# Kernel optimization log

Hardware: AMD Instinct MI355X
Metric: run time of the kernel (lower is better)

The kernel has to match this reference:

```python
import jax, jax.numpy as jnp
import numpy as np

N = 50000      # nodes
E = 1000000    # edges
NF = 5         # node_features
EF = 2         # edge_features
RS = 128       # rnn_size
RES = 32       # rnn_edge_size
H = 4          # heads
C = 16         # out_features
FIN = RS + RES # GAT in_channels
NEG_SLOPE = 0.2


def lstm_step(x, h, c, Wih, Whh, bih, bhh):
    # Single-step LSTM (torch gate order: i, f, g, o)
    g = x @ Wih.T + h @ Whh.T + bih + bhh
    i, f, gg, o = jnp.split(g, 4, axis=-1)
    i = jax.nn.sigmoid(i); f = jax.nn.sigmoid(f)
    gg = jnp.tanh(gg); o = jax.nn.sigmoid(o)
    c2 = f * c + i * gg
    return o * jnp.tanh(c2), c2


def setup_inputs() -> dict:
    key = jax.random.key(0)
    ks = jax.random.split(key, 20)
    p = lambda k, shape: (jax.random.normal(k, shape) * 0.1).astype(jnp.float32)
    return dict(
        x=jax.random.normal(ks[0], (N, NF), jnp.float32),
        edge_index=jax.random.randint(ks[1], (2, E), 0, N),
        edge_attr=jax.random.normal(ks[2], (E, EF), jnp.float32),
        h_node_h=p(ks[3], (N, RS)), h_node_c=p(ks[4], (N, RS)),
        h_edge_h=p(ks[5], (E, RES)), h_edge_c=p(ks[6], (E, RES)),
        Wih_n=p(ks[7], (4 * RS, NF)), Whh_n=p(ks[8], (4 * RS, RS)),
        bih_n=p(ks[9], (4 * RS,)), bhh_n=p(ks[10], (4 * RS,)),
        Wih_e=p(ks[11], (4 * RES, EF)), Whh_e=p(ks[12], (4 * RES, RES)),
        bih_e=p(ks[13], (4 * RES,)), bhh_e=p(ks[14], (4 * RES,)),
        W_gat=p(ks[15], (FIN, H * C)),
        att_src=p(ks[16], (H, C)), att_dst=p(ks[17], (H, C)),
        bias_gat=p(ks[18], (C,)),
    )


def reference(x, edge_index, edge_attr, h_node_h, h_node_c, h_edge_h, h_edge_c,
              Wih_n, Whh_n, bih_n, bhh_n, Wih_e, Whh_e, bih_e, bhh_e,
              W_gat, att_src, att_dst, bias_gat):
    n = x.shape[0]
    # --- edge history encoder: per-edge LSTM step + scatter-mean to dst nodes ---
    he, ce = lstm_step(edge_attr, h_edge_h, h_edge_c, Wih_e, Whh_e, bih_e, bhh_e)
    dst0 = edge_index[1]
    esum = jax.ops.segment_sum(he, dst0, num_segments=n)
    deg = jax.ops.segment_sum(jnp.ones((he.shape[0], 1), he.dtype), dst0, num_segments=n)
    edge_enc = esum / jnp.maximum(deg, 1.0)            # [N, RES]
    # --- node history encoder: per-node LSTM step ---
    hn, cn = lstm_step(x, h_node_h, h_node_c, Wih_n, Whh_n, bih_n, bhh_n)
    feat = jnp.concatenate([hn, edge_enc], axis=-1)    # [N, FIN]
    # --- GATConv (PyG v1 style, add_self_loops=True, concat=False) ---
    xl = (feat @ W_gat).reshape(n, H, C)               # [N, H, C]
    a_src = jnp.einsum('nhc,hc->nh', xl, att_src)
    a_dst = jnp.einsum('nhc,hc->nh', xl, att_dst)
    loops = jnp.arange(n)
    src = jnp.concatenate([edge_index[0], loops])
    dst = jnp.concatenate([edge_index[1], loops])
    alpha = jax.nn.leaky_relu(a_src[src] + a_dst[dst], NEG_SLOPE)  # [E+N, H]
    m = jax.ops.segment_max(alpha, dst, num_segments=n)
    ea = jnp.exp(alpha - m[dst])
    s = jax.ops.segment_sum(ea, dst, num_segments=n)
    w = ea / s[dst]                                     # segment softmax over dst
    out = jax.ops.segment_sum(xl[src] * w[:, :, None], dst, num_segments=n)  # [N,H,C]
    out = out.mean(axis=1) + bias_gat                   # concat=False -> head mean
    return (out, hn, cn, he, ce)
```

## Files before the change

kernel.cpp:

```cpp
#include <hip/hip_runtime.h>

#define CAP 128

typedef __attribute__((ext_vector_type(8))) short bf16x8;
typedef __attribute__((ext_vector_type(4))) float f32x4;

__device__ __forceinline__ float sigf(float x) {
    return __builtin_amdgcn_rcpf(1.0f + __expf(-x));
}
__device__ __forceinline__ float tanhfast(float x) {
    return 2.0f * __builtin_amdgcn_rcpf(1.0f + __expf(-2.0f * x)) - 1.0f;
}
__device__ __forceinline__ short bfr(float f) {
    unsigned u = __float_as_uint(f);
    unsigned r = (u + 0x7FFFu + ((u >> 16) & 1u)) >> 16;
    return (short)r;
}
__device__ __forceinline__ float bf2f(unsigned short u) {
    return __uint_as_float(((unsigned)u) << 16);
}
__device__ __forceinline__ bf16x8 cvt8(const float* p) {
    const float4* q = (const float4*)p;
    float4 u = q[0], v = q[1];
    bf16x8 r;
    r[0]=bfr(u.x); r[1]=bfr(u.y); r[2]=bfr(u.z); r[3]=bfr(u.w);
    r[4]=bfr(v.x); r[5]=bfr(v.y); r[6]=bfr(v.z); r[7]=bfr(v.w);
    return r;
}

__global__ void convert_kernel(
    const float* __restrict__ Whh_n, const float* __restrict__ Wih_n,
    const float* __restrict__ bih_n, const float* __restrict__ bhh_n,
    const float* __restrict__ Whh_e, const float* __restrict__ Wih_e,
    const float* __restrict__ bih_e, const float* __restrict__ bhh_e,
    const float* __restrict__ Wgat,
    unsigned short* __restrict__ WnF, unsigned short* __restrict__ WeF,
    unsigned short* __restrict__ WgF, int* __restrict__ cnt, int N)
{
    int i = blockIdx.x * 256 + threadIdx.x;
    if (i < N) cnt[i] = 0;
    if (i < 512 * 160) {
        int j = i & 7, unit = i >> 3;
        int lane = unit & 63, tk = unit >> 6;
        int t = tk / 5, k4 = tk - t * 5;
        int r = t * 16 + (lane & 15);
        int k = k4 * 32 + (lane >> 4) * 8 + j;
        float v = (k < 128) ? Whh_n[r * 128 + k]
                : (k < 133) ? Wih_n[r * 5 + (k - 128)]
                : (k == 133) ? (bih_n[r] + bhh_n[r]) : 0.f;
        WnF[i] = (unsigned short)bfr(v);
    }
    if (i < 128 * 64) {
        int j = i & 7, unit = i >> 3;
        int lane = unit & 63, ts = unit >> 6;
        int t = ts >> 1, s = ts & 1;
        int r = t * 16 + (lane & 15);
        int k = s * 32 + (lane >> 4) * 8 + j;
        float v = (k < 32) ? Whh_e[r * 32 + k]
                : (k < 34) ? Wih_e[r * 2 + (k - 32)]
                : (k == 34) ? (bih_e[r] + bhh_e[r]) : 0.f;
        WeF[i] = (unsigned short)bfr(v);
    }
    if (i < 64 * 160) {
        int j = i & 7, unit = i >> 3;
        int lane = unit & 63, tk = unit >> 6;
        int t = tk / 5, k4 = tk - t * 5;
        int r = t * 16 + (lane & 15);
        int k = k4 * 32 + (lane >> 4) * 8 + j;
        WgF[i] = (unsigned short)bfr(Wgat[k * 64 + r]);
    }
}

__global__ void csr_fill_kernel(const int* __restrict__ dst, int* __restrict__ cnt,
                                int* __restrict__ eid, int E)
{
    int e = blockIdx.x * blockDim.x + threadIdx.x;
    if (e >= E) return;
    int d = dst[e];
    int k = atomicAdd(cnt + d, 1);
    if (k < CAP) eid[(size_t)d * CAP + k] = e;
}

__global__ __launch_bounds__(256) void edge_lstm_mfma(
    const float* __restrict__ eattr, const float* __restrict__ h_in, const float* __restrict__ c_in,
    const unsigned short* __restrict__ WeF,
    float* __restrict__ he_out, float* __restrict__ ce_out, int E)
{
    const int lane = threadIdx.x & 63, wave = threadIdx.x >> 6;
    const int lr = lane & 15, lg = lane >> 4;
    const int T = E >> 4;
    const int wstride = gridDim.x * 4;
    const int wid = blockIdx.x * 4 + wave;
    if (wid >= T) return;
    const bf16x8* Wv = (const bf16x8*)WeF;
    bf16x8 wa0[8], wa1[8];
    #pragma unroll
    for (int t = 0; t < 8; ++t) {
        wa0[t] = Wv[(t * 2 + 0) * 64 + lane];
        wa1[t] = Wv[(t * 2 + 1) * 64 + lane];
    }
    const int jb0 = lg * 4, jb1 = 16 + lg * 4;
    float4 ph0, ph1; f32x4 pc0, pc1; float2 pea;
    {
        const int e0 = wid * 16 + lr;
        const float4* hp = (const float4*)(h_in + (size_t)e0 * 32);
        ph0 = hp[lg * 2]; ph1 = hp[lg * 2 + 1];
        pc0 = *(const f32x4*)(c_in + (size_t)e0 * 32 + jb0);
        pc1 = *(const f32x4*)(c_in + (size_t)e0 * 32 + jb1);
        pea = *(const float2*)(eattr + (size_t)e0 * 2);
    }
    for (int t = wid; t < T; t += wstride) {
        const float4 h0 = ph0, h1 = ph1; const f32x4 c0v = pc0, c1v = pc1; const float2 ea = pea;
        const int edge = t * 16 + lr;
        const int tn = t + wstride;
        if (tn < T) {
            const int en = tn * 16 + lr;
            const float4* hp = (const float4*)(h_in + (size_t)en * 32);
            ph0 = hp[lg * 2]; ph1 = hp[lg * 2 + 1];
            pc0 = *(const f32x4*)(c_in + (size_t)en * 32 + jb0);
            pc1 = *(const f32x4*)(c_in + (size_t)en * 32 + jb1);
            pea = *(const float2*)(eattr + (size_t)en * 2);
        }
        bf16x8 b0;
        b0[0]=bfr(h0.x); b0[1]=bfr(h0.y); b0[2]=bfr(h0.z); b0[3]=bfr(h0.w);
        b0[4]=bfr(h1.x); b0[5]=bfr(h1.y); b0[6]=bfr(h1.z); b0[7]=bfr(h1.w);
        bf16x8 b1 = {0,0,0,0,0,0,0,0};
        if (lg == 0) {
            b1[0] = bfr(ea.x); b1[1] = bfr(ea.y); b1[2] = (short)0x3F80;
        }
        f32x4 acc[8];
        #pragma unroll
        for (int tt = 0; tt < 8; ++tt) {
            f32x4 v = {0, 0, 0, 0};
            v = __builtin_amdgcn_mfma_f32_16x16x32_bf16(wa0[tt], b0, v, 0, 0, 0);
            v = __builtin_amdgcn_mfma_f32_16x16x32_bf16(wa1[tt], b1, v, 0, 0, 0);
            acc[tt] = v;
        }
        #pragma unroll
        for (int u = 0; u < 2; ++u) {
            const int jb = u ? jb1 : jb0;
            const f32x4 cold = u ? c1v : c0v;
            f32x4 cres, hres;
            #pragma unroll
            for (int q = 0; q < 4; ++q) {
                float gi = acc[u][q],     gf = acc[u + 2][q];
                float gg = acc[u + 4][q], go = acc[u + 6][q];
                float c2 = sigf(gf) * cold[q] + sigf(gi) * tanhfast(gg);
                cres[q] = c2;
                hres[q] = sigf(go) * tanhfast(c2);
            }
            __builtin_nontemporal_store(cres, (f32x4*)(ce_out + (size_t)edge * 32 + jb));
            *(f32x4*)(he_out + (size_t)edge * 32 + jb) = hres;
        }
    }
}

__global__ __launch_bounds__(256) void node_lstm_mfma(
    const float* __restrict__ x, const float* __restrict__ h_in, const float* __restrict__ c_in,
    const unsigned short* __restrict__ WnF,
    float* __restrict__ hn_out, float* __restrict__ cn_out, int N)
{
    const int lane = threadIdx.x & 63, wave = threadIdx.x >> 6;
    const int n0 = blockIdx.x * 64 + wave * 16;
    if (n0 >= N) return;
    const int lr = lane & 15, lg = lane >> 4;
    const int node = n0 + lr;
    bf16x8 b[5];
    const float* hp = h_in + (size_t)node * 128 + lg * 8;
    b[0] = cvt8(hp); b[1] = cvt8(hp + 32); b[2] = cvt8(hp + 64); b[3] = cvt8(hp + 96);
    bf16x8 bx = {0,0,0,0,0,0,0,0};
    if (lg == 0) {
        const float* xp = x + (size_t)node * 5;
        bx[0]=bfr(xp[0]); bx[1]=bfr(xp[1]); bx[2]=bfr(xp[2]); bx[3]=bfr(xp[3]); bx[4]=bfr(xp[4]);
        bx[5] = (short)0x3F80;
    }
    b[4] = bx;
    const bf16x8* Wv = (const bf16x8*)WnF;
    f32x4 acc[32];
    #pragma unroll
    for (int t = 0; t < 32; ++t) {
        const bf16x8* ap = Wv + t * 320 + lane;
        f32x4 v = {0, 0, 0, 0};
        #pragma unroll
        for (int k4 = 0; k4 < 5; ++k4)
            v = __builtin_amdgcn_mfma_f32_16x16x32_bf16(ap[k4 * 64], b[k4], v, 0, 0, 0);
        acc[t] = v;
    }
    #pragma unroll
    for (int u = 0; u < 8; ++u) {
        const int jb = u * 16 + lg * 4;
        f32x4 cold = *(const f32x4*)(c_in + (size_t)node * 128 + jb);
        f32x4 cres, hres;
        #pragma unroll
        for (int q = 0; q < 4; ++q) {
            float gi = acc[u][q],        gf = acc[u + 8][q];
            float gg = acc[u + 16][q],   go = acc[u + 24][q];
            float c2 = sigf(gf) * cold[q] + sigf(gi) * tanhfast(gg);
            cres[q] = c2;
            hres[q] = sigf(go) * tanhfast(c2);
        }
        __builtin_nontemporal_store(cres, (f32x4*)(cn_out + (size_t)node * 128 + jb));
        *(f32x4*)(hn_out + (size_t)node * 128 + jb) = hres;
    }
}

__global__ __launch_bounds__(256) void enc_gatxl_kernel(
    const int* __restrict__ cnt, const int* __restrict__ eid, const float* __restrict__ he,
    const float* __restrict__ hn, const unsigned short* __restrict__ WgF,
    const float* __restrict__ attS, const float* __restrict__ attD,
    unsigned short* __restrict__ xlb, float* __restrict__ asrc, float* __restrict__ adst, int N)
{
    __shared__ float encs[64 * 36];
    const int lane = threadIdx.x & 63, wave = threadIdx.x >> 6;
    const int nbase = blockIdx.x * 64 + wave * 16;
    if (nbase >= N) return;
    const int half = lane >> 5, hl = lane & 31;
    const int g4 = hl >> 3, l8 = hl & 7;
    for (int t = 0; t < 16; t += 2) {
        const int node = nbase + t + half;
        const int c = cnt[node];
        const int m = min(c, CAP);
        const int* el = eid + (size_t)node * CAP;
        f32x4 acc = {0, 0, 0, 0};
        for (int i = g4; i < m; i += 4)
            acc += *(const f32x4*)(he + (size_t)el[i] * 32 + l8 * 4);
        #pragma unroll
        for (int off = 8; off <= 16; off <<= 1) {
            acc[0] += __shfl_xor(acc[0], off);
            acc[1] += __shfl_xor(acc[1], off);
            acc[2] += __shfl_xor(acc[2], off);
            acc[3] += __shfl_xor(acc[3], off);
        }
        if (g4 == 0) {
            float inv = 1.0f / fmaxf((float)c, 1.0f);
            f32x4 r; r[0]=acc[0]*inv; r[1]=acc[1]*inv; r[2]=acc[2]*inv; r[3]=acc[3]*inv;
            *(f32x4*)(&encs[(wave * 16 + t + half) * 36 + l8 * 4]) = r;
        }
    }
    const int lr = lane & 15, lg = lane >> 4;
    const int node = nbase + lr;
    bf16x8 b[5];
    const float* hp = hn + (size_t)node * 128 + lg * 8;
    b[0] = cvt8(hp); b[1] = cvt8(hp + 32); b[2] = cvt8(hp + 64); b[3] = cvt8(hp + 96);
    b[4] = cvt8(&encs[(wave * 16 + lr) * 36 + lg * 8]);
    const bf16x8* Wv = (const bf16x8*)WgF;
    #pragma unroll
    for (int t = 0; t < 4; ++t) {
        const bf16x8* ap = Wv + t * 320 + lane;
        f32x4 v = {0, 0, 0, 0};
        #pragma unroll
        for (int k4 = 0; k4 < 5; ++k4)
            v = __builtin_amdgcn_mfma_f32_16x16x32_bf16(ap[k4 * 64], b[k4], v, 0, 0, 0);
        ushort4 pk;
        pk.x = (unsigned short)bfr(v[0]); pk.y = (unsigned short)bfr(v[1]);
        pk.z = (unsigned short)bfr(v[2]); pk.w = (unsigned short)bfr(v[3]);
        *(ushort4*)(xlb + (size_t)node * 64 + t * 16 + lg * 4) = pk;
        const f32x4 ws = *(const f32x4*)(attS + t * 16 + lg * 4);
        const f32x4 wd = *(const f32x4*)(attD + t * 16 + lg * 4);
        float p1 = v[0]*ws[0] + v[1]*ws[1] + v[2]*ws[2] + v[3]*ws[3];
        float p2 = v[0]*wd[0] + v[1]*wd[1] + v[2]*wd[2] + v[3]*wd[3];
        p1 += __shfl_xor(p1, 16); p2 += __shfl_xor(p2, 16);
        p1 += __shfl_xor(p1, 32); p2 += __shfl_xor(p2, 32);
        if (lg == 0) {
            asrc[(size_t)node * 4 + t] = p1;
            adst[(size_t)node * 4 + t] = p2;
        }
    }
}

__global__ __launch_bounds__(256) void gat_node_kernel(
    const int* __restrict__ cnt, const int* __restrict__ eid,
    const int* __restrict__ src_idx,
    const float* __restrict__ asrc, const float* __restrict__ adst,
    const unsigned short* __restrict__ xlb, const float* __restrict__ bias,
    float* __restrict__ out, int N)
{
    const int wid = (blockIdx.x * blockDim.x + threadIdx.x) >> 6;
    const int lane = threadIdx.x & 63;
    if (wid >= N) return;
    const int n = wid;
    const int m = min(cnt[n], CAP);
    const int h = lane >> 4, c16 = lane & 15;
    const int nslot = (m + 15) >> 4;
    const float ad = adst[n * 4 + h];
    float aself = asrc[n * 4 + h] + ad;
    aself = aself > 0.f ? aself : 0.2f * aself;
    const int* el = eid + (size_t)n * CAP;
    int   ss[8];
    float aa[8];
    float mx = aself;
    #pragma unroll
    for (int k = 0; k < 8; ++k) {
        if (k >= nslot) break;
        int i = k * 16 + c16;
        if (i < m) {
            int s = src_idx[el[i]];
            float a = asrc[s * 4 + h] + ad;
            a = a > 0.f ? a : 0.2f * a;
            ss[k] = s; aa[k] = a;
            mx = fmaxf(mx, a);
        } else { ss[k] = 0; aa[k] = -1e30f; }
    }
    #pragma unroll
    for (int off = 1; off < 16; off <<= 1) mx = fmaxf(mx, __shfl_xor(mx, off));
    float ea[8];
    float p = 0.f;
    #pragma unroll
    for (int k = 0; k < 8; ++k) {
        if (k >= nslot) break;
        ea[k] = __expf(aa[k] - mx);
        p += ea[k];
    }
    #pragma unroll
    for (int off = 1; off < 16; off <<= 1) p += __shfl_xor(p, off);
    float eself = __expf(aself - mx);
    float sacc = eself + p;
    float oacc = eself * bf2f(xlb[(size_t)n * 64 + lane]);
    const int grp = lane & 48;
    #pragma unroll
    for (int k = 0; k < 8; ++k) {
        if (k >= nslot) break;
        const int lim = min(16, m - k * 16);
        #pragma unroll 4
        for (int cc = 0; cc < lim; ++cc) {
            int srcl = grp | cc;
            float w = __shfl(ea[k], srcl);
            int   s = __shfl(ss[k], srcl);
            oacc += w * bf2f(xlb[(size_t)s * 64 + lane]);
        }
    }
    float r = oacc / sacc;
    r += __shfl_xor(r, 16);
    r += __shfl_xor(r, 32);
    if (lane < 16) out[(size_t)n * 16 + lane] = 0.25f * r + bias[lane];
}

extern "C" void kernel_launch(void* const* d_in, const int* in_sizes, int n_in,
                              void* d_out, int out_size, void* d_ws, size_t ws_size,
                              hipStream_t stream)
{
    const float* x     = (const float*)d_in[0];
    const int*   ei    = (const int*)  d_in[1];
    const float* eattr = (const float*)d_in[2];
    const float* hn_h  = (const float*)d_in[3];
    const float* hn_c  = (const float*)d_in[4];
    const float* he_h  = (const float*)d_in[5];
    const float* he_c  = (const float*)d_in[6];
    const float* Wih_n = (const float*)d_in[7];
    const float* Whh_n = (const float*)d_in[8];
    const float* bih_n = (const float*)d_in[9];
    const float* bhh_n = (const float*)d_in[10];
    const float* Wih_e = (const float*)d_in[11];
    const float* Whh_e = (const float*)d_in[12];
    const float* bih_e = (const float*)d_in[13];
    const float* bhh_e = (const float*)d_in[14];
    const float* W_gat = (const float*)d_in[15];
    const float* attS  = (const float*)d_in[16];
    const float* attD  = (const float*)d_in[17];
    const float* biasG = (const float*)d_in[18];

    const int N = in_sizes[0] / 5;
    const int E = in_sizes[2] / 2;

    float* out = (float*)d_out;
    float* hn  = out + (size_t)N * 16;
    float* cn  = hn  + (size_t)N * 128;
    float* he  = cn  + (size_t)N * 128;
    float* ce  = he  + (size_t)E * 32;

    char* p = (char*)d_ws;
    size_t off = 0;
    auto take = [&](size_t bytes) -> void* {
        void* r = p + off;
        off = (off + bytes + 255) & ~(size_t)255;
        return r;
    };
    int*   cnt  = (int*)  take((size_t)N * 4);
    int*   eid  = (int*)  take((size_t)N * CAP * 4);
    unsigned short* xlb = (unsigned short*)take((size_t)N * 64 * 2);
    float* asrc = (float*)take((size_t)N * 4 * 4);
    float* adst = (float*)take((size_t)N * 4 * 4);
    unsigned short* WnF = (unsigned short*)take(512 * 160 * 2);
    unsigned short* WeF = (unsigned short*)take(128 * 64 * 2);
    unsigned short* WgF = (unsigned short*)take(64 * 160 * 2);

    convert_kernel<<<(512 * 160 + 255) / 256, 256, 0, stream>>>(
        Whh_n, Wih_n, bih_n, bhh_n, Whh_e, Wih_e, bih_e, bhh_e, W_gat,
        WnF, WeF, WgF, cnt, N);
    csr_fill_kernel<<<(E + 255) / 256, 256, 0, stream>>>(ei + E, cnt, eid, E);
    edge_lstm_mfma<<<2048, 256, 0, stream>>>(
        eattr, he_h, he_c, WeF, he, ce, E);
    node_lstm_mfma<<<(N + 63) / 64, 256, 0, stream>>>(
        x, hn_h, hn_c, WnF, hn, cn, N);
    enc_gatxl_kernel<<<(N + 63) / 64, 256, 0, stream>>>(
        cnt, eid, he, hn, WgF, attS, attD, xlb, asrc, adst, N);
    gat_node_kernel<<<(N + 3) / 4, 256, 0, stream>>>(
        cnt, eid, ei, asrc, adst, xlb, biasG, out, N);
}
```

Baseline: 380.1 us.

## Fuse CSR fill, edge LSTM and node LSTM into one block-specialized kernel

Merges the CSR-fill atomics, the edge LSTM and the node LSTM into a single launch. The 4096 blocks are partitioned by block index: three of every four run edge LSTM work, and the remaining blocks are split between the node LSTM and the CSR fill, so these independent streams can overlap on the GPU. The node weight layout is permuted so that the four gates for each hidden slice sit next to each other. This lets the node LSTM compute and consume four accumulators at a time instead of holding 32, which lowers register pressure. The goal is to remove launch gaps and tail idling between the three kernels. The cost is that block types may be imbalanced and the fused kernel's register footprint is set by its heaviest branch.

```diff
diff --git a/kernel.cpp b/kernel.cpp
--- a/kernel.cpp
+++ b/kernel.cpp
@@ -42,8 +42,8 @@
     if (i < 512 * 160) {
         int j = i & 7, unit = i >> 3;
         int lane = unit & 63, tk = unit >> 6;
-        int t = tk / 5, k4 = tk - t * 5;
-        int r = t * 16 + (lane & 15);
+        int tp = tk / 5, k4 = tk - tp * 5;
+        int r = (tp & 3) * 128 + (tp >> 2) * 16 + (lane & 15);
         int k = k4 * 32 + (lane >> 4) * 8 + j;
         float v = (k < 128) ? Whh_n[r * 128 + k]
                 : (k < 133) ? Wih_n[r * 5 + (k - 128)]
@@ -71,136 +71,136 @@
     }
 }
 
-__global__ void csr_fill_kernel(const int* __restrict__ dst, int* __restrict__ cnt,
-                                int* __restrict__ eid, int E)
-{
-    int e = blockIdx.x * blockDim.x + threadIdx.x;
-    if (e >= E) return;
-    int d = dst[e];
-    int k = atomicAdd(cnt + d, 1);
-    if (k < CAP) eid[(size_t)d * CAP + k] = e;
-}
-
-__global__ __launch_bounds__(256) void edge_lstm_mfma(
-    const float* __restrict__ eattr, const float* __restrict__ h_in, const float* __restrict__ c_in,
+__global__ __launch_bounds__(256) void phase1_kernel(
+    const float* __restrict__ eattr, const float* __restrict__ he_h, const float* __restrict__ he_c,
     const unsigned short* __restrict__ WeF,
-    float* __restrict__ he_out, float* __restrict__ ce_out, int E)
-{
+    float* __restrict__ he_out, float* __restrict__ ce_out, int E,
+    const float* __restrict__ x, const float* __restrict__ hn_h, const float* __restrict__ hn_c,
+    const unsigned short* __restrict__ WnF,
+    float* __restrict__ hn_out, float* __restrict__ cn_out, int N,
+    const int* __restrict__ dst, int* __restrict__ cnt, int* __restrict__ eid)
+{
+    const int B = blockIdx.x;
     const int lane = threadIdx.x & 63, wave = threadIdx.x >> 6;
     const int lr = lane & 15, lg = lane >> 4;
-    const int T = E >> 4;
-    const int wstride = gridDim.x * 4;
-    const int wid = blockIdx.x * 4 + wave;
-    if (wid >= T) return;
-    const bf16x8* Wv = (const bf16x8*)WeF;
-    bf16x8 wa0[8], wa1[8];
-    #pragma unroll
-    for (int t = 0; t < 8; ++t) {
-        wa0[t] = Wv[(t * 2 + 0) * 64 + lane];
-        wa1[t] = Wv[(t * 2 + 1) * 64 + lane];
-    }
-    const int jb0 = lg * 4, jb1 = 16 + lg * 4;
-    float4 ph0, ph1; f32x4 pc0, pc1; float2 pea;
-    {
-        const int e0 = wid * 16 + lr;
-        const float4* hp = (const float4*)(h_in + (size_t)e0 * 32);
-        ph0 = hp[lg * 2]; ph1 = hp[lg * 2 + 1];
-        pc0 = *(const f32x4*)(c_in + (size_t)e0 * 32 + jb0);
-        pc1 = *(const f32x4*)(c_in + (size_t)e0 * 32 + jb1);
-        pea = *(const float2*)(eattr + (size_t)e0 * 2);
-    }
-    for (int t = wid; t < T; t += wstride) {
-        const float4 h0 = ph0, h1 = ph1; const f32x4 c0v = pc0, c1v = pc1; const float2 ea = pea;
-        const int edge = t * 16 + lr;
-        const int tn = t + wstride;
-        if (tn < T) {
-            const int en = tn * 16 + lr;
-            const float4* hp = (const float4*)(h_in + (size_t)en * 32);
+    const int r4 = B & 3;
+
+    if (r4 != 3) {
+        const int eb = (B >> 2) * 3 + r4;
+        const int T = E >> 4;
+        const int wstride = 3072 * 4;
+        const int wid = eb * 4 + wave;
+        if (wid >= T) return;
+        const bf16x8* Wv = (const bf16x8*)WeF;
+        bf16x8 wa0[8], wa1[8];
+        #pragma unroll
+        for (int t = 0; t < 8; ++t) {
+            wa0[t] = Wv[(t * 2 + 0) * 64 + lane];
+            wa1[t] = Wv[(t * 2 + 1) * 64 + lane];
+        }
+        const int jb0 = lg * 4, jb1 = 16 + lg * 4;
+        float4 ph0, ph1; f32x4 pc0, pc1; float2 pea;
+        {
+            const int e0 = wid * 16 + lr;
+            const float4* hp = (const float4*)(he_h + (size_t)e0 * 32);
             ph0 = hp[lg * 2]; ph1 = hp[lg * 2 + 1];
-            pc0 = *(const f32x4*)(c_in + (size_t)en * 32 + jb0);
-            pc1 = *(const f32x4*)(c_in + (size_t)en * 32 + jb1);
-            pea = *(const float2*)(eattr + (size_t)en * 2);
-        }
-        bf16x8 b0;
-        b0[0]=bfr(h0.x); b0[1]=bfr(h0.y); b0[2]=bfr(h0.z); b0[3]=bfr(h0.w);
-        b0[4]=bfr(h1.x); b0[5]=bfr(h1.y); b0[6]=bfr(h1.z); b0[7]=bfr(h1.w);
-        bf16x8 b1 = {0,0,0,0,0,0,0,0};
-        if (lg == 0) {
-            b1[0] = bfr(ea.x); b1[1] = bfr(ea.y); b1[2] = (short)0x3F80;
-        }
-        f32x4 acc[8];
-        #pragma unroll
-        for (int tt = 0; tt < 8; ++tt) {
-            f32x4 v = {0, 0, 0, 0};
-            v = __builtin_amdgcn_mfma_f32_16x16x32_bf16(wa0[tt], b0, v, 0, 0, 0);
-            v = __builtin_amdgcn_mfma_f32_16x16x32_bf16(wa1[tt], b1, v, 0, 0, 0);
-            acc[tt] = v;
-        }
-        #pragma unroll
-        for (int u = 0; u < 2; ++u) {
-            const int jb = u ? jb1 : jb0;
-            const f32x4 cold = u ? c1v : c0v;
-            f32x4 cres, hres;
+            pc0 = *(const f32x4*)(he_c + (size_t)e0 * 32 + jb0);
+            pc1 = *(const f32x4*)(he_c + (size_t)e0 * 32 + jb1);
+            pea = *(const float2*)(eattr + (size_t)e0 * 2);
+        }
+        for (int t = wid; t < T; t += wstride) {
+            const float4 h0 = ph0, h1 = ph1; const f32x4 c0v = pc0, c1v = pc1; const float2 ea = pea;
+            const int edge = t * 16 + lr;
+            const int tn = t + wstride;
+            if (tn < T) {
+                const int en = tn * 16 + lr;
+                const float4* hp = (const float4*)(he_h + (size_t)en * 32);
+                ph0 = hp[lg * 2]; ph1 = hp[lg * 2 + 1];
+                pc0 = *(const f32x4*)(he_c + (size_t)en * 32 + jb0);
+                pc1 = *(const f32x4*)(he_c + (size_t)en * 32 + jb1);
+                pea = *(const float2*)(eattr + (size_t)en * 2);
+            }
+            bf16x8 b0;
+            b0[0]=bfr(h0.x); b0[1]=bfr(h0.y); b0[2]=bfr(h0.z); b0[3]=bfr(h0.w);
+            b0[4]=bfr(h1.x); b0[5]=bfr(h1.y); b0[6]=bfr(h1.z); b0[7]=bfr(h1.w);
+            bf16x8 b1 = {0,0,0,0,0,0,0,0};
+            if (lg == 0) {
+                b1[0] = bfr(ea.x); b1[1] = bfr(ea.y); b1[2] = (short)0x3F80;
+            }
+            f32x4 acc[8];
             #pragma unroll
-            for (int q = 0; q < 4; ++q) {
-                float gi = acc[u][q],     gf = acc[u + 2][q];
-                float gg = acc[u + 4][q], go = acc[u + 6][q];
-                float c2 = sigf(gf) * cold[q] + sigf(gi) * tanhfast(gg);
-                cres[q] = c2;
-                hres[q] = sigf(go) * tanhfast(c2);
-            }
-            __builtin_nontemporal_store(cres, (f32x4*)(ce_out + (size_t)edge * 32 + jb));
-            *(f32x4*)(he_out + (size_t)edge * 32 + jb) = hres;
-        }
-    }
-}
-
-__global__ __launch_bounds__(256) void node_lstm_mfma(
-    const float* __restrict__ x, const float* __restrict__ h_in, const float* __restrict__ c_in,
-    const unsigned short* __restrict__ WnF,
-    float* __restrict__ hn_out, float* __restrict__ cn_out, int N)
-{
-    const int lane = threadIdx.x & 63, wave = threadIdx.x >> 6;
-    const int n0 = blockIdx.x * 64 + wave * 16;
-    if (n0 >= N) return;
-    const int lr = lane & 15, lg = lane >> 4;
-    const int node = n0 + lr;
-    bf16x8 b[5];
-    const float* hp = h_in + (size_t)node * 128 + lg * 8;
-    b[0] = cvt8(hp); b[1] = cvt8(hp + 32); b[2] = cvt8(hp + 64); b[3] = cvt8(hp + 96);
-    bf16x8 bx = {0,0,0,0,0,0,0,0};
-    if (lg == 0) {
-        const float* xp = x + (size_t)node * 5;
-        bx[0]=bfr(xp[0]); bx[1]=bfr(xp[1]); bx[2]=bfr(xp[2]); bx[3]=bfr(xp[3]); bx[4]=bfr(xp[4]);
-        bx[5] = (short)0x3F80;
-    }
-    b[4] = bx;
-    const bf16x8* Wv = (const bf16x8*)WnF;
-    f32x4 acc[32];
-    #pragma unroll
-    for (int t = 0; t < 32; ++t) {
-        const bf16x8* ap = Wv + t * 320 + lane;
-        f32x4 v = {0, 0, 0, 0};
-        #pragma unroll
-        for (int k4 = 0; k4 < 5; ++k4)
-            v = __builtin_amdgcn_mfma_f32_16x16x32_bf16(ap[k4 * 64], b[k4], v, 0, 0, 0);
-        acc[t] = v;
-    }
-    #pragma unroll
-    for (int u = 0; u < 8; ++u) {
-        const int jb = u * 16 + lg * 4;
-        f32x4 cold = *(const f32x4*)(c_in + (size_t)node * 128 + jb);
-        f32x4 cres, hres;
-        #pragma unroll
-        for (int q = 0; q < 4; ++q) {
-            float gi = acc[u][q],        gf = acc[u + 8][q];
-            float gg = acc[u + 16][q],   go = acc[u + 24][q];
-            float c2 = sigf(gf) * cold[q] + sigf(gi) * tanhfast(gg);
-            cres[q] = c2;
-            hres[q] = sigf(go) * tanhfast(c2);
-        }
-        __builtin_nontemporal_store(cres, (f32x4*)(cn_out + (size_t)node * 128 + jb));
-        *(f32x4*)(hn_out + (size_t)node * 128 + jb) = hres;
+            for (int tt = 0; tt < 8; ++tt) {
+                f32x4 v = {0, 0, 0, 0};
+                v = __builtin_amdgcn_mfma_f32_16x16x32_bf16(wa0[tt], b0, v, 0, 0, 0);
+                v = __builtin_amdgcn_mfma_f32_16x16x32_bf16(wa1[tt], b1, v, 0, 0, 0);
+                acc[tt] = v;
+            }
+            #pragma unroll
+            for (int u = 0; u < 2; ++u) {
+                const int jb = u ? jb1 : jb0;
+                const f32x4 cold = u ? c1v : c0v;
+                f32x4 cres, hres;
+                #pragma unroll
+                for (int q = 0; q < 4; ++q) {
+                    float gi = acc[u][q],     gf = acc[u + 2][q];
+                    float gg = acc[u + 4][q], go = acc[u + 6][q];
+                    float c2 = sigf(gf) * cold[q] + sigf(gi) * tanhfast(gg);
+                    cres[q] = c2;
+                    hres[q] = sigf(go) * tanhfast(c2);
+                }
+                __builtin_nontemporal_store(cres, (f32x4*)(ce_out + (size_t)edge * 32 + jb));
+                *(f32x4*)(he_out + (size_t)edge * 32 + jb) = hres;
+            }
+        }
+    } else if ((B & 7) == 3) {
+        const int nb = B >> 3;
+        const int NG = N >> 4;
+        const int wstride = 512 * 4;
+        const bf16x8* Wv = (const bf16x8*)WnF;
+        for (int gidx = nb * 4 + wave; gidx < NG; gidx += wstride) {
+            const int node = gidx * 16 + lr;
+            bf16x8 b[5];
+            const float* hp = hn_h + (size_t)node * 128 + lg * 8;
+            b[0] = cvt8(hp); b[1] = cvt8(hp + 32); b[2] = cvt8(hp + 64); b[3] = cvt8(hp + 96);
+            bf16x8 bx = {0,0,0,0,0,0,0,0};
+            if (lg == 0) {
+                const float* xp = x + (size_t)node * 5;
+                bx[0]=bfr(xp[0]); bx[1]=bfr(xp[1]); bx[2]=bfr(xp[2]); bx[3]=bfr(xp[3]); bx[4]=bfr(xp[4]);
+                bx[5] = (short)0x3F80;
+            }
+            b[4] = bx;
+            #pragma unroll
+            for (int u = 0; u < 8; ++u) {
+                f32x4 acc[4];
+                #pragma unroll
+                for (int g = 0; g < 4; ++g) {
+                    const bf16x8* ap = Wv + (u * 4 + g) * 320 + lane;
+                    f32x4 v = {0, 0, 0, 0};
+                    #pragma unroll
+                    for (int k4 = 0; k4 < 5; ++k4)
+                        v = __builtin_amdgcn_mfma_f32_16x16x32_bf16(ap[k4 * 64], b[k4], v, 0, 0, 0);
+                    acc[g] = v;
+                }
+                const int jb = u * 16 + lg * 4;
+                f32x4 cold = *(const f32x4*)(hn_c + (size_t)node * 128 + jb);
+                f32x4 cres, hres;
+                #pragma unroll
+                for (int q = 0; q < 4; ++q) {
+                    float c2 = sigf(acc[1][q]) * cold[q] + sigf(acc[0][q]) * tanhfast(acc[2][q]);
+                    cres[q] = c2;
+                    hres[q] = sigf(acc[3][q]) * tanhfast(c2);
+                }
+                __builtin_nontemporal_store(cres, (f32x4*)(cn_out + (size_t)node * 128 + jb));
+                *(f32x4*)(hn_out + (size_t)node * 128 + jb) = hres;
+            }
+        }
+    } else {
+        const int cb = B >> 3;
+        for (int e = cb * 256 + threadIdx.x; e < E; e += 512 * 256) {
+            int d = dst[e];
+            int k = atomicAdd(cnt + d, 1);
+            if (k < CAP) eid[(size_t)d * CAP + k] = e;
+        }
     }
 }
 
@@ -387,11 +387,10 @@
     convert_kernel<<<(512 * 160 + 255) / 256, 256, 0, stream>>>(
         Whh_n, Wih_n, bih_n, bhh_n, Whh_e, Wih_e, bih_e, bhh_e, W_gat,
         WnF, WeF, WgF, cnt, N);
-    csr_fill_kernel<<<(E + 255) / 256, 256, 0, stream>>>(ei + E, cnt, eid, E);
-    edge_lstm_mfma<<<2048, 256, 0, stream>>>(
-        eattr, he_h, he_c, WeF, he, ce, E);
-    node_lstm_mfma<<<(N + 63) / 64, 256, 0, stream>>>(
-        x, hn_h, hn_c, WnF, hn, cn, N);
+    phase1_kernel<<<4096, 256, 0, stream>>>(
+        eattr, he_h, he_c, WeF, he, ce, E,
+        x, hn_h, hn_c, WnF, hn, cn, N,
+        ei + E, cnt, eid);
     enc_gatxl_kernel<<<(N + 63) / 64, 256, 0, stream>>>(
         cnt, eid, he, hn, WgF, attS, attD, xlb, asrc, adst, N);
     gat_node_kernel<<<(N + 3) / 4, 256, 0, stream>>>(
```

New measurement: 930.1 us. +144.7%, slower.

## Coalesce edge LSTM I/O via LDS transpose and interleave node LSTM gates

Applied to the files above, without the earlier changes.

The edge LSTM now assigns one 16-edge tile per wave and loads h/c contiguously as a wave-wide block. The h tile and the gate results are transposed through shared memory, so global loads and stores are fully coalesced instead of strided per-edge accesses. The grid-stride prefetch loop is replaced by a launch over all tiles with a 4-block occupancy hint. The node LSTM weights are reordered so each output chunk's four gates are computed together, which shrinks live accumulators from 32 to 4 registers at the cost of LDS traffic and extra block launches.

```diff
diff --git a/kernel.cpp b/kernel.cpp
--- a/kernel.cpp
+++ b/kernel.cpp
@@ -42,8 +42,8 @@
     if (i < 512 * 160) {
         int j = i & 7, unit = i >> 3;
         int lane = unit & 63, tk = unit >> 6;
-        int t = tk / 5, k4 = tk - t * 5;
-        int r = t * 16 + (lane & 15);
+        int tp = tk / 5, k4 = tk - tp * 5;
+        int r = (tp & 3) * 128 + (tp >> 2) * 16 + (lane & 15);
         int k = k4 * 32 + (lane >> 4) * 8 + j;
         float v = (k < 128) ? Whh_n[r * 128 + k]
                 : (k < 133) ? Wih_n[r * 5 + (k - 128)]
@@ -81,17 +81,31 @@
     if (k < CAP) eid[(size_t)d * CAP + k] = e;
 }
 
-__global__ __launch_bounds__(256) void edge_lstm_mfma(
+__global__ __launch_bounds__(256, 4) void edge_lstm_mfma(
     const float* __restrict__ eattr, const float* __restrict__ h_in, const float* __restrict__ c_in,
     const unsigned short* __restrict__ WeF,
     float* __restrict__ he_out, float* __restrict__ ce_out, int E)
 {
+    __shared__ float Gall[4][16 * 132];
+    __shared__ unsigned short Hall[4][16 * 40];
     const int lane = threadIdx.x & 63, wave = threadIdx.x >> 6;
     const int lr = lane & 15, lg = lane >> 4;
-    const int T = E >> 4;
-    const int wstride = gridDim.x * 4;
-    const int wid = blockIdx.x * 4 + wave;
-    if (wid >= T) return;
+    const int tile = blockIdx.x * 4 + wave;
+    if (tile * 16 >= E) return;
+    float* G = Gall[wave];
+    unsigned short* H = Hall[wave];
+
+    const size_t dwbase = (size_t)tile * 512;
+    const f32x4 hA = *(const f32x4*)(h_in + dwbase + lane * 4);
+    const f32x4 hB = *(const f32x4*)(h_in + dwbase + 256 + lane * 4);
+    const f32x4 cA = *(const f32x4*)(c_in + dwbase + lane * 4);
+    const f32x4 cB = *(const f32x4*)(c_in + dwbase + 256 + lane * 4);
+    float ea0 = 0.f, ea1 = 0.f;
+    if (lg == 0) {
+        ea0 = eattr[(size_t)(tile * 16 + lr) * 2];
+        ea1 = eattr[(size_t)(tile * 16 + lr) * 2 + 1];
+    }
+
     const bf16x8* Wv = (const bf16x8*)WeF;
     bf16x8 wa0[8], wa1[8];
     #pragma unroll
@@ -99,59 +113,56 @@
         wa0[t] = Wv[(t * 2 + 0) * 64 + lane];
         wa1[t] = Wv[(t * 2 + 1) * 64 + lane];
     }
-    const int jb0 = lg * 4, jb1 = 16 + lg * 4;
-    float4 ph0, ph1; f32x4 pc0, pc1; float2 pea;
+
     {
-        const int e0 = wid * 16 + lr;
-        const float4* hp = (const float4*)(h_in + (size_t)e0 * 32);
-        ph0 = hp[lg * 2]; ph1 = hp[lg * 2 + 1];
-        pc0 = *(const f32x4*)(c_in + (size_t)e0 * 32 + jb0);
-        pc1 = *(const f32x4*)(c_in + (size_t)e0 * 32 + jb1);
-        pea = *(const float2*)(eattr + (size_t)e0 * 2);
-    }
-    for (int t = wid; t < T; t += wstride) {
-        const float4 h0 = ph0, h1 = ph1; const f32x4 c0v = pc0, c1v = pc1; const float2 ea = pea;
-        const int edge = t * 16 + lr;
-        const int tn = t + wstride;
-        if (tn < T) {
-            const int en = tn * 16 + lr;
-            const float4* hp = (const float4*)(h_in + (size_t)en * 32);
-            ph0 = hp[lg * 2]; ph1 = hp[lg * 2 + 1];
-            pc0 = *(const f32x4*)(c_in + (size_t)en * 32 + jb0);
-            pc1 = *(const f32x4*)(c_in + (size_t)en * 32 + jb1);
-            pea = *(const float2*)(eattr + (size_t)en * 2);
-        }
-        bf16x8 b0;
-        b0[0]=bfr(h0.x); b0[1]=bfr(h0.y); b0[2]=bfr(h0.z); b0[3]=bfr(h0.w);
-        b0[4]=bfr(h1.x); b0[5]=bfr(h1.y); b0[6]=bfr(h1.z); b0[7]=bfr(h1.w);
-        bf16x8 b1 = {0,0,0,0,0,0,0,0};
-        if (lg == 0) {
-            b1[0] = bfr(ea.x); b1[1] = bfr(ea.y); b1[2] = (short)0x3F80;
-        }
-        f32x4 acc[8];
+        const int e = lane >> 3, c4 = (lane & 7) * 4;
+        ushort4 pa, pb;
+        pa.x = (unsigned short)bfr(hA[0]); pa.y = (unsigned short)bfr(hA[1]);
+        pa.z = (unsigned short)bfr(hA[2]); pa.w = (unsigned short)bfr(hA[3]);
+        pb.x = (unsigned short)bfr(hB[0]); pb.y = (unsigned short)bfr(hB[1]);
+        pb.z = (unsigned short)bfr(hB[2]); pb.w = (unsigned short)bfr(hB[3]);
+        *(ushort4*)(H + e * 40 + c4)       = pa;
+        *(ushort4*)(H + (8 + e) * 40 + c4) = pb;
+    }
+    bf16x8 b0 = *(const bf16x8*)(H + lr * 40 + lg * 8);
+    bf16x8 b1 = {0,0,0,0,0,0,0,0};
+    if (lg == 0) {
+        b1[0] = bfr(ea0); b1[1] = bfr(ea1); b1[2] = (short)0x3F80;
+    }
+
+    f32x4 acc[8];
+    #pragma unroll
+    for (int t = 0; t < 8; ++t) {
+        f32x4 v = {0, 0, 0, 0};
+        v = __builtin_amdgcn_mfma_f32_16x16x32_bf16(wa0[t], b0, v, 0, 0, 0);
+        v = __builtin_amdgcn_mfma_f32_16x16x32_bf16(wa1[t], b1, v, 0, 0, 0);
+        acc[t] = v;
+    }
+
+    #pragma unroll
+    for (int u = 0; u < 8; ++u) {
+        const int col = (u >> 1) * 32 + (u & 1) * 16 + lg * 4;
+        *(f32x4*)(G + lr * 132 + col) = acc[u];
+    }
+
+    const int e = lane >> 3, jq = (lane & 7) * 4;
+    #pragma unroll
+    for (int part = 0; part < 2; ++part) {
+        const float* gr = G + (part * 8 + e) * 132;
+        const f32x4 gi = *(const f32x4*)(gr + jq);
+        const f32x4 gf = *(const f32x4*)(gr + 32 + jq);
+        const f32x4 gg = *(const f32x4*)(gr + 64 + jq);
+        const f32x4 go = *(const f32x4*)(gr + 96 + jq);
+        const f32x4 cold = part ? cB : cA;
+        f32x4 cres, hres;
         #pragma unroll
-        for (int tt = 0; tt < 8; ++tt) {
-            f32x4 v = {0, 0, 0, 0};
-            v = __builtin_amdgcn_mfma_f32_16x16x32_bf16(wa0[tt], b0, v, 0, 0, 0);
-            v = __builtin_amdgcn_mfma_f32_16x16x32_bf16(wa1[tt], b1, v, 0, 0, 0);
-            acc[tt] = v;
-        }
-        #pragma unroll
-        for (int u = 0; u < 2; ++u) {
-            const int jb = u ? jb1 : jb0;
-            const f32x4 cold = u ? c1v : c0v;
-            f32x4 cres, hres;
-            #pragma unroll
-            for (int q = 0; q < 4; ++q) {
-                float gi = acc[u][q],     gf = acc[u + 2][q];
-                float gg = acc[u + 4][q], go = acc[u + 6][q];
-                float c2 = sigf(gf) * cold[q] + sigf(gi) * tanhfast(gg);
-                cres[q] = c2;
-                hres[q] = sigf(go) * tanhfast(c2);
-            }
-            __builtin_nontemporal_store(cres, (f32x4*)(ce_out + (size_t)edge * 32 + jb));
-            *(f32x4*)(he_out + (size_t)edge * 32 + jb) = hres;
-        }
+        for (int q = 0; q < 4; ++q) {
+            float c2 = sigf(gf[q]) * cold[q] + sigf(gi[q]) * tanhfast(gg[q]);
+            cres[q] = c2;
+            hres[q] = sigf(go[q]) * tanhfast(c2);
+        }
+        __builtin_nontemporal_store(cres, (f32x4*)(ce_out + dwbase + part * 256 + lane * 4));
+        *(f32x4*)(he_out + dwbase + part * 256 + lane * 4) = hres;
     }
 }
 
@@ -161,10 +172,10 @@
     float* __restrict__ hn_out, float* __restrict__ cn_out, int N)
 {
     const int lane = threadIdx.x & 63, wave = threadIdx.x >> 6;
-    const int n0 = blockIdx.x * 64 + wave * 16;
-    if (n0 >= N) return;
+    const int nbase = blockIdx.x * 64 + wave * 16;
+    if (nbase >= N) return;
     const int lr = lane & 15, lg = lane >> 4;
-    const int node = n0 + lr;
+    const int node = nbase + lr;
     bf16x8 b[5];
     const float* hp = h_in + (size_t)node * 128 + lg * 8;
     b[0] = cvt8(hp); b[1] = cvt8(hp + 32); b[2] = cvt8(hp + 64); b[3] = cvt8(hp + 96);
@@ -176,28 +187,26 @@
     }
     b[4] = bx;
     const bf16x8* Wv = (const bf16x8*)WnF;
-    f32x4 acc[32];
-    #pragma unroll
-    for (int t = 0; t < 32; ++t) {
-        const bf16x8* ap = Wv + t * 320 + lane;
-        f32x4 v = {0, 0, 0, 0};
+    #pragma unroll
+    for (int u = 0; u < 8; ++u) {
+        f32x4 acc[4];
         #pragma unroll
-        for (int k4 = 0; k4 < 5; ++k4)
-            v = __builtin_amdgcn_mfma_f32_16x16x32_bf16(ap[k4 * 64], b[k4], v, 0, 0, 0);
-        acc[t] = v;
-    }
-    #pragma unroll
-    for (int u = 0; u < 8; ++u) {
+        for (int g = 0; g < 4; ++g) {
+            const bf16x8* ap = Wv + (u * 4 + g) * 320 + lane;
+            f32x4 v = {0, 0, 0, 0};
+            #pragma unroll
+            for (int k4 = 0; k4 < 5; ++k4)
+                v = __builtin_amdgcn_mfma_f32_16x16x32_bf16(ap[k4 * 64], b[k4], v, 0, 0, 0);
+            acc[g] = v;
+        }
         const int jb = u * 16 + lg * 4;
         f32x4 cold = *(const f32x4*)(c_in + (size_t)node * 128 + jb);
         f32x4 cres, hres;
         #pragma unroll
         for (int q = 0; q < 4; ++q) {
-            float gi = acc[u][q],        gf = acc[u + 8][q];
-            float gg = acc[u + 16][q],   go = acc[u + 24][q];
-            float c2 = sigf(gf) * cold[q] + sigf(gi) * tanhfast(gg);
+            float c2 = sigf(acc[1][q]) * cold[q] + sigf(acc[0][q]) * tanhfast(acc[2][q]);
             cres[q] = c2;
-            hres[q] = sigf(go) * tanhfast(c2);
+            hres[q] = sigf(acc[3][q]) * tanhfast(c2);
         }
         __builtin_nontemporal_store(cres, (f32x4*)(cn_out + (size_t)node * 128 + jb));
         *(f32x4*)(hn_out + (size_t)node * 128 + jb) = hres;
@@ -388,7 +397,7 @@
         Whh_n, Wih_n, bih_n, bhh_n, Whh_e, Wih_e, bih_e, bhh_e, W_gat,
         WnF, WeF, WgF, cnt, N);
     csr_fill_kernel<<<(E + 255) / 256, 256, 0, stream>>>(ei + E, cnt, eid, E);
-    edge_lstm_mfma<<<2048, 256, 0, stream>>>(
+    edge_lstm_mfma<<<(E + 63) / 64, 256, 0, stream>>>(
         eattr, he_h, he_c, WeF, he, ce, E);
     node_lstm_mfma<<<(N + 63) / 64, 256, 0, stream>>>(
         x, hn_h, hn_c, WnF, hn, cn, N);
```

New measurement: 367.2 us. 3.4% less time.
